# Optimization experiments

Hardware: AMD Instinct MI355X
Metric: run time of the kernel (lower is better)

## Reference

```python
import jax, jax.numpy as jnp
import numpy as np

B, L, H = 16, 2048, 768
V, D = 30000, 64


def setup_inputs() -> dict:
    key = jax.random.key(0)
    k1, k2, k3, k4 = jax.random.split(key, 4)
    bert_x = jax.random.normal(k1, (B, L, H), dtype=jnp.float32)
    x = jax.random.randint(k2, (B, L), 0, V, dtype=jnp.int64)
    ae = jax.random.normal(k3, (V, D), dtype=jnp.float32)
    w = jax.random.normal(k4, (D, D), dtype=jnp.float32)
    return {"bert_x": bert_x, "x": x, "ae": ae, "w": w}


def reference(bert_x, x, ae, w):
    # E[b,i] = ae[x[b,i]]  -> [B, L, D]
    E = ae[x]
    # fac[b,i,j] = E[b,i] @ w @ E[b,j]   (bilinear pairwise score)
    scores = jnp.einsum('bid,de,bje->bij', E, w, E)
    Lseq = bert_x.shape[1]
    i = jnp.arange(Lseq, dtype=bert_x.dtype)[:, None]
    j = jnp.arange(Lseq, dtype=bert_x.dtype)[None, :]
    # strictly-causal weight (i+1)/(j+1) for i < j, zero elsewhere
    coef = jnp.where(i < j, (i + 1.0) / (j + 1.0), 0.0).astype(bert_x.dtype)
    # res[:, j] = bert_x[:, j] + sum_{i<j} bert_x[:, i] * coef[i,j] * fac[b,i,j]
    res = bert_x + jnp.einsum('bij,bih->bjh', scores * coef, bert_x)
    return res
```

## Files before the change

kernel.cpp:

```cpp
#include <hip/hip_runtime.h>

#define Bb 16
#define Ll 2048
#define Hh 768
#define Dd 64
#define Cc 64
#define HC 64
#define NT (Hh / HC)
#define NCH (Ll / Cc)
#define NG 6

typedef __attribute__((ext_vector_type(8))) short bf16x8;
typedef __attribute__((ext_vector_type(4))) float f32x4;

__device__ __forceinline__ short f2bf(float f) {
  union { float f; unsigned u; } c;
  c.f = f;
  unsigned r = (c.u + 0x7FFFu + ((c.u >> 16) & 1u)) >> 16;
  return (short)r;
}
__device__ __forceinline__ unsigned pack2(float a, float b) {
  return (unsigned)(unsigned short)f2bf(a) | ((unsigned)(unsigned short)f2bf(b) << 16);
}
__device__ __forceinline__ float bf2f(unsigned short s) {
  union { unsigned u; float f; } c;
  c.u = ((unsigned)s) << 16;
  return c.f;
}

__device__ __forceinline__ void sync_lds() {
  asm volatile("s_waitcnt lgkmcnt(0)\n\ts_barrier" ::: "memory");
}

__global__ __launch_bounds__(512) void prep_kernel(const int* __restrict__ x,
                                                   const float* __restrict__ ae,
                                                   const float* __restrict__ w,
                                                   const float* __restrict__ bx,
                                                   short* __restrict__ Eg,
                                                   short* __restrict__ scTg,
                                                   short* __restrict__ Sch) {
  const int tid = threadIdx.x;
  const int wv = tid >> 6, lane = tid & 63, quad = lane >> 4, lq = lane & 15;
  const int mt = wv >> 1, np = wv & 1;
  const int b = blockIdx.x >> 5, ch = blockIdx.x & 31;
  const size_t gb = (size_t)blockIdx.x * 4096;
  __shared__ short pool[4 * 4096];
  short* sE  = pool;
  short* sWT = pool + 4096;
  short* sF  = pool + 8192;
  short* sFT = pool + 12288;

  {
    const int i = tid >> 3, seg = tid & 7;
    const int idx = x[b * Ll + ch * Cc + i];
    const float4* aer = (const float4*)(ae + (size_t)idx * Dd) + seg * 2;
    const float4 a0 = aer[0], a1 = aer[1];
    uint4 p;
    p.x = pack2(a0.x, a0.y); p.y = pack2(a0.z, a0.w);
    p.z = pack2(a1.x, a1.y); p.w = pack2(a1.z, a1.w);
    *(uint4*)&sE[i * 64 + ((seg ^ (i & 7)) << 3)] = p;
    *(uint4*)(Eg + gb + i * 64 + seg * 8) = p;
    const float4* wr = (const float4*)w;
#pragma unroll
    for (int q = 0; q < 2; ++q) {
      const int fl = q * 512 + tid;
      const int d = fl >> 4, es = (fl & 15) * 4;
      const float4 v = wr[fl];
      const float vv[4] = {v.x, v.y, v.z, v.w};
#pragma unroll
      for (int c = 0; c < 4; ++c) {
        const int e = es + c;
        sWT[e * 64 + (((d >> 3) ^ (e & 7)) << 3) + (d & 7)] = f2bf(vv[c]);
      }
    }
  }
  __syncthreads();

  const int rm = mt * 16 + lq;
  bf16x8 aE[2], aW[2];
#pragma unroll
  for (int ks = 0; ks < 2; ++ks) {
    const int blk = ((ks * 4 + quad) ^ (rm & 7)) << 3;
    aE[ks] = *(const bf16x8*)&sE[rm * 64 + blk];
    aW[ks] = *(const bf16x8*)&sWT[rm * 64 + blk];
  }

#pragma unroll
  for (int t = 0; t < 2; ++t) {
    const int nt = np * 2 + t;
    const int rn = nt * 16 + lq;
    f32x4 accF = {}, accT = {};
#pragma unroll
    for (int ks = 0; ks < 2; ++ks) {
      const int blk = ((ks * 4 + quad) ^ (rn & 7)) << 3;
      const bf16x8 bW = *(const bf16x8*)&sWT[rn * 64 + blk];
      const bf16x8 bE = *(const bf16x8*)&sE[rn * 64 + blk];
      accF = __builtin_amdgcn_mfma_f32_16x16x32_bf16(aE[ks], bW, accF, 0, 0, 0);
      accT = __builtin_amdgcn_mfma_f32_16x16x32_bf16(aW[ks], bE, accT, 0, 0, 0);
    }
#pragma unroll
    for (int r = 0; r < 4; ++r) {
      const int i = mt * 16 + quad * 4 + r;
      const int e = nt * 16 + lq;
      sF[i * 64 + (((e >> 3) ^ (i & 7)) << 3) + (e & 7)] = f2bf(accF[r]);
      const int d2 = mt * 16 + quad * 4 + r;
      const int i2 = nt * 16 + lq;
      sFT[d2 * 64 + (((i2 >> 3) ^ (d2 & 7)) << 3) + (i2 & 7)] = f2bf(accT[r]);
    }
  }
  __syncthreads();

  const int ip = tid & 31, hg = tid >> 5;
  float4 rGa[2], rGb[2];
  auto load_G = [&](int g) {
    const float* xr = bx + ((size_t)(b * Ll) + ch * Cc + 2 * ip) * Hh + g * 128 + hg * 8;
    rGa[0] = *(const float4*)(xr);
    rGa[1] = *(const float4*)(xr + 4);
    rGb[0] = *(const float4*)(xr + Hh);
    rGb[1] = *(const float4*)(xr + Hh + 4);
  };
  load_G(0);

#pragma unroll
  for (int t = 0; t < 2; ++t) {
    const int nt = np * 2 + t;
    const int rn = nt * 16 + lq;
    f32x4 acc = {};
#pragma unroll
    for (int ks = 0; ks < 2; ++ks) {
      const int blk = ((ks * 4 + quad) ^ (rn & 7)) << 3;
      const bf16x8 bF = *(const bf16x8*)&sF[rn * 64 + blk];
      acc = __builtin_amdgcn_mfma_f32_16x16x32_bf16(aE[ks], bF, acc, 0, 0, 0);
    }
#pragma unroll
    for (int r = 0; r < 4; ++r) {
      const int j = mt * 16 + quad * 4 + r;
      const int i = nt * 16 + lq;
      scTg[gb + j * 64 + i] = f2bf(i < j ? acc[r] : 0.f);
    }
  }

  bf16x8 bFT[4][2];
#pragma unroll
  for (int nt = 0; nt < 4; ++nt) {
    const int rn = nt * 16 + lq;
#pragma unroll
    for (int ks = 0; ks < 2; ++ks) {
      const int blk = ((ks * 4 + quad) ^ (rn & 7)) << 3;
      bFT[nt][ks] = *(const bf16x8*)&sFT[rn * 64 + blk];
    }
  }

  short* So = Sch + (size_t)blockIdx.x * (Hh * Dd);
#pragma unroll 2
  for (int g = 0; g < NG; ++g) {
    short* gbuf = pool + (g & 1) * 8192;
    {
      const float s0 = (float)(ch * Cc + 2 * ip + 1), s1 = (float)(ch * Cc + 2 * ip + 2);
      const float A[8] = {rGa[0].x, rGa[0].y, rGa[0].z, rGa[0].w,
                          rGa[1].x, rGa[1].y, rGa[1].z, rGa[1].w};
      const float Bv[8] = {rGb[0].x, rGb[0].y, rGb[0].z, rGb[0].w,
                           rGb[1].x, rGb[1].y, rGb[1].z, rGb[1].w};
#pragma unroll
      for (int e = 0; e < 8; ++e) {
        const int hl = hg * 8 + e;
        const int sa = hl * 64 + (((ip >> 2) ^ (hl & 7)) << 3) + 2 * (ip & 3);
        *(unsigned*)&gbuf[sa] = pack2(A[e] * s0, Bv[e] * s1);
      }
    }
    if (g + 1 < NG) load_G(g + 1);
    sync_lds();
    const int rh = wv * 16 + lq;
    bf16x8 aG[2];
#pragma unroll
    for (int ks = 0; ks < 2; ++ks) {
      const int blk = ((ks * 4 + quad) ^ (rh & 7)) << 3;
      aG[ks] = *(const bf16x8*)&gbuf[rh * 64 + blk];
    }
#pragma unroll
    for (int nt = 0; nt < 4; ++nt) {
      f32x4 acc = {};
#pragma unroll
      for (int ks = 0; ks < 2; ++ks)
        acc = __builtin_amdgcn_mfma_f32_16x16x32_bf16(aG[ks], bFT[nt][ks], acc, 0, 0, 0);
#pragma unroll
      for (int r = 0; r < 4; ++r) {
        const int h = g * 128 + wv * 16 + quad * 4 + r;
        So[h * 64 + nt * 16 + lq] = f2bf(acc[r]);
      }
    }
  }
}

__global__ __launch_bounds__(256) void prefix_kernel(short* __restrict__ Sch) {
  const int b = blockIdx.x / 48;
  const int v = (blockIdx.x % 48) * 256 + threadIdx.x;
  uint2* base = (uint2*)(Sch + (size_t)b * NCH * (Hh * Dd)) + v;
  const int stride = Hh * Dd / 4;
  uint2 va[NCH];
#pragma unroll
  for (int s = 0; s < NCH; ++s) va[s] = base[s * stride];
  float4 acc = {0.f, 0.f, 0.f, 0.f};
#pragma unroll
  for (int s = 0; s < NCH; ++s) {
    uint2 o;
    o.x = pack2(acc.x, acc.y);
    o.y = pack2(acc.z, acc.w);
    base[s * stride] = o;
    acc.x += bf2f((unsigned short)(va[s].x & 0xffffu));
    acc.y += bf2f((unsigned short)(va[s].x >> 16));
    acc.z += bf2f((unsigned short)(va[s].y & 0xffffu));
    acc.w += bf2f((unsigned short)(va[s].y >> 16));
  }
}

__global__ __launch_bounds__(256) void scan_kernel(const float* __restrict__ bx,
                                                   const short* __restrict__ Eg,
                                                   const short* __restrict__ scTg,
                                                   const short* __restrict__ STg,
                                                   float* __restrict__ out) {
  const int s = blockIdx.x;
  const int tile = s >> 9;
  const int bc = s & 511;
  const int b = bc >> 5, ch = bc & 31;
  const int tid = threadIdx.x;
  const int w = tid >> 6, lane = tid & 63, quad = lane >> 4, lq = lane & 15;
  const int ip = tid & 31, hg = tid >> 5;
  const int rj = w * 16 + lq;

  __shared__ short sGT[64 * 64];

  float4 rGa[2], rGb[2];
  {
    const float* xr = bx + ((size_t)(b * Ll) + ch * Cc + 2 * ip) * Hh + tile * HC + hg * 8;
    rGa[0] = *(const float4*)(xr);
    rGa[1] = *(const float4*)(xr + 4);
    rGb[0] = *(const float4*)(xr + Hh);
    rGb[1] = *(const float4*)(xr + Hh + 4);
  }
  bf16x8 aC1[2], aC2[2];
  {
    const size_t tb = (size_t)bc * 4096;
#pragma unroll
    for (int ks = 0; ks < 2; ++ks) {
      const int o = rj * 64 + (ks * 4 + quad) * 8;
      aC1[ks] = *(const bf16x8*)(scTg + tb + o);
      aC2[ks] = *(const bf16x8*)(Eg + tb + o);
    }
  }
  bf16x8 stF[4][2];
  {
    const short* Sp = STg + (size_t)bc * (Hh * Dd);
#pragma unroll
    for (int ht = 0; ht < 4; ++ht) {
      const int h = tile * HC + ht * 16 + lq;
#pragma unroll
      for (int ks = 0; ks < 2; ++ks)
        stF[ht][ks] = *(const bf16x8*)(Sp + h * 64 + (ks * 4 + quad) * 8);
    }
  }

  {
    const float s0 = (float)(ch * Cc + 2 * ip + 1), s1 = (float)(ch * Cc + 2 * ip + 2);
    const float A[8] = {rGa[0].x, rGa[0].y, rGa[0].z, rGa[0].w,
                        rGa[1].x, rGa[1].y, rGa[1].z, rGa[1].w};
    const float Bv[8] = {rGb[0].x, rGb[0].y, rGb[0].z, rGb[0].w,
                         rGb[1].x, rGb[1].y, rGb[1].z, rGb[1].w};
#pragma unroll
    for (int e = 0; e < 8; ++e) {
      const int hl = hg * 8 + e;
      const int sa = hl * 64 + (((ip >> 2) ^ (hl & 7)) << 3) + 2 * (ip & 3);
      *(unsigned*)&sGT[sa] = pack2(A[e] * s0, Bv[e] * s1);
    }
  }
  sync_lds();

#pragma unroll
  for (int ht = 0; ht < 4; ++ht) {
    const int rh = ht * 16 + lq;
    f32x4 accO = {};
#pragma unroll
    for (int ks = 0; ks < 2; ++ks) {
      const int blk = ((ks * 4 + quad) ^ (rh & 7)) << 3;
      const bf16x8 gv = *(const bf16x8*)&sGT[rh * 64 + blk];
      accO = __builtin_amdgcn_mfma_f32_16x16x32_bf16(aC1[ks], gv, accO, 0, 0, 0);
      accO = __builtin_amdgcn_mfma_f32_16x16x32_bf16(aC2[ks], stF[ht][ks], accO, 0, 0, 0);
    }
#pragma unroll
    for (int r = 0; r < 4; ++r) {
      const int gj = ch * Cc + w * 16 + quad * 4 + r;
      const size_t off = ((size_t)(b * Ll) + gj) * Hh + tile * HC + ht * 16 + lq;
      out[off] = bx[off] + accO[r] * (1.0f / (float)(gj + 1));
    }
  }
}

extern "C" void kernel_launch(void* const* d_in, const int* in_sizes, int n_in,
                              void* d_out, int out_size, void* d_ws, size_t ws_size,
                              hipStream_t stream) {
  (void)in_sizes; (void)n_in; (void)out_size; (void)ws_size;
  const float* bx = (const float*)d_in[0];
  const int* x = (const int*)d_in[1];
  const float* ae = (const float*)d_in[2];
  const float* w = (const float*)d_in[3];
  float* out = (float*)d_out;
  short* Eg = (short*)d_ws;
  short* scTg = Eg + (size_t)512 * 4096;
  short* Sch = scTg + (size_t)512 * 4096;

  prep_kernel<<<Bb * NCH, 512, 0, stream>>>(x, ae, w, bx, Eg, scTg, Sch);
  prefix_kernel<<<Bb * 48, 256, 0, stream>>>(Sch);
  scan_kernel<<<NT * Bb * NCH, 256, 0, stream>>>(bx, Eg, scTg, Sch, out);
}
```

Measured before the change: 263.9 us.

## Process four H-tiles per scan block with double-buffered LDS and prefetch

Each scan_kernel block now loops over four consecutive 64-wide H tiles instead of one. The per-chunk A-operand fragments (scTg, Eg) are loaded once and reused across the tiles. The next tile's bert_x and prefix-state loads are issued while the current tile computes, with the LDS staging buffer alternating between two copies. This cuts the grid by four and removes redundant operand loads, but it lowers block-level parallelism and raises register and LDS use per block.

```diff
diff --git a/kernel.cpp b/kernel.cpp
--- a/kernel.cpp
+++ b/kernel.cpp
@@ -9,6 +9,8 @@
 #define NT (Hh / HC)
 #define NCH (Ll / Cc)
 #define NG 6
+#define TG 4
+#define NTG (NT / TG)
 
 typedef __attribute__((ext_vector_type(8))) short bf16x8;
 typedef __attribute__((ext_vector_type(4))) float f32x4;
@@ -220,7 +222,7 @@
                                                    const short* __restrict__ STg,
                                                    float* __restrict__ out) {
   const int s = blockIdx.x;
-  const int tile = s >> 9;
+  const int tg = s >> 9;
   const int bc = s & 511;
   const int b = bc >> 5, ch = bc & 31;
   const int tid = threadIdx.x;
@@ -228,70 +230,82 @@
   const int ip = tid & 31, hg = tid >> 5;
   const int rj = w * 16 + lq;
 
-  __shared__ short sGT[64 * 64];
+  __shared__ short sGT[2][64 * 64];
+
+  bf16x8 aC1[2], aC2[2];
+  {
+    const size_t tb = (size_t)bc * 4096;
+#pragma unroll
+    for (int ks = 0; ks < 2; ++ks) {
+      const int o = rj * 64 + (ks * 4 + quad) * 8;
+      aC1[ks] = *(const bf16x8*)(scTg + tb + o);
+      aC2[ks] = *(const bf16x8*)(Eg + tb + o);
+    }
+  }
+  const short* Sp = STg + (size_t)bc * (Hh * Dd);
 
   float4 rGa[2], rGb[2];
-  {
-    const float* xr = bx + ((size_t)(b * Ll) + ch * Cc + 2 * ip) * Hh + tile * HC + hg * 8;
+  bf16x8 stF[4][2];
+  auto load_G = [&](int tl) {
+    const float* xr = bx + ((size_t)(b * Ll) + ch * Cc + 2 * ip) * Hh + tl * HC + hg * 8;
     rGa[0] = *(const float4*)(xr);
     rGa[1] = *(const float4*)(xr + 4);
     rGb[0] = *(const float4*)(xr + Hh);
     rGb[1] = *(const float4*)(xr + Hh + 4);
-  }
-  bf16x8 aC1[2], aC2[2];
-  {
-    const size_t tb = (size_t)bc * 4096;
-#pragma unroll
-    for (int ks = 0; ks < 2; ++ks) {
-      const int o = rj * 64 + (ks * 4 + quad) * 8;
-      aC1[ks] = *(const bf16x8*)(scTg + tb + o);
-      aC2[ks] = *(const bf16x8*)(Eg + tb + o);
-    }
-  }
-  bf16x8 stF[4][2];
-  {
-    const short* Sp = STg + (size_t)bc * (Hh * Dd);
+  };
+  auto load_S = [&](int tl) {
 #pragma unroll
     for (int ht = 0; ht < 4; ++ht) {
-      const int h = tile * HC + ht * 16 + lq;
+      const int h = tl * HC + ht * 16 + lq;
 #pragma unroll
       for (int ks = 0; ks < 2; ++ks)
         stF[ht][ks] = *(const bf16x8*)(Sp + h * 64 + (ks * 4 + quad) * 8);
     }
-  }
-
-  {
-    const float s0 = (float)(ch * Cc + 2 * ip + 1), s1 = (float)(ch * Cc + 2 * ip + 2);
-    const float A[8] = {rGa[0].x, rGa[0].y, rGa[0].z, rGa[0].w,
-                        rGa[1].x, rGa[1].y, rGa[1].z, rGa[1].w};
-    const float Bv[8] = {rGb[0].x, rGb[0].y, rGb[0].z, rGb[0].w,
-                         rGb[1].x, rGb[1].y, rGb[1].z, rGb[1].w};
-#pragma unroll
-    for (int e = 0; e < 8; ++e) {
-      const int hl = hg * 8 + e;
-      const int sa = hl * 64 + (((ip >> 2) ^ (hl & 7)) << 3) + 2 * (ip & 3);
-      *(unsigned*)&sGT[sa] = pack2(A[e] * s0, Bv[e] * s1);
-    }
-  }
-  sync_lds();
-
-#pragma unroll
-  for (int ht = 0; ht < 4; ++ht) {
-    const int rh = ht * 16 + lq;
-    f32x4 accO = {};
-#pragma unroll
-    for (int ks = 0; ks < 2; ++ks) {
-      const int blk = ((ks * 4 + quad) ^ (rh & 7)) << 3;
-      const bf16x8 gv = *(const bf16x8*)&sGT[rh * 64 + blk];
-      accO = __builtin_amdgcn_mfma_f32_16x16x32_bf16(aC1[ks], gv, accO, 0, 0, 0);
-      accO = __builtin_amdgcn_mfma_f32_16x16x32_bf16(aC2[ks], stF[ht][ks], accO, 0, 0, 0);
-    }
-#pragma unroll
-    for (int r = 0; r < 4; ++r) {
-      const int gj = ch * Cc + w * 16 + quad * 4 + r;
-      const size_t off = ((size_t)(b * Ll) + gj) * Hh + tile * HC + ht * 16 + lq;
-      out[off] = bx[off] + accO[r] * (1.0f / (float)(gj + 1));
-    }
+  };
+
+  load_G(tg * TG);
+  load_S(tg * TG);
+
+  const float s0 = (float)(ch * Cc + 2 * ip + 1), s1 = (float)(ch * Cc + 2 * ip + 2);
+
+#pragma unroll
+  for (int t = 0; t < TG; ++t) {
+    const int tl = tg * TG + t;
+    short* gbuf = sGT[t & 1];
+    {
+      const float A[8] = {rGa[0].x, rGa[0].y, rGa[0].z, rGa[0].w,
+                          rGa[1].x, rGa[1].y, rGa[1].z, rGa[1].w};
+      const float Bv[8] = {rGb[0].x, rGb[0].y, rGb[0].z, rGb[0].w,
+                           rGb[1].x, rGb[1].y, rGb[1].z, rGb[1].w};
+#pragma unroll
+      for (int e = 0; e < 8; ++e) {
+        const int hl = hg * 8 + e;
+        const int sa = hl * 64 + (((ip >> 2) ^ (hl & 7)) << 3) + 2 * (ip & 3);
+        *(unsigned*)&gbuf[sa] = pack2(A[e] * s0, Bv[e] * s1);
+      }
+    }
+    if (t + 1 < TG) load_G(tl + 1);
+    sync_lds();
+
+#pragma unroll
+    for (int ht = 0; ht < 4; ++ht) {
+      const int rh = ht * 16 + lq;
+      f32x4 accO = {};
+#pragma unroll
+      for (int ks = 0; ks < 2; ++ks) {
+        const int blk = ((ks * 4 + quad) ^ (rh & 7)) << 3;
+        const bf16x8 gv = *(const bf16x8*)&gbuf[rh * 64 + blk];
+        accO = __builtin_amdgcn_mfma_f32_16x16x32_bf16(aC1[ks], gv, accO, 0, 0, 0);
+        accO = __builtin_amdgcn_mfma_f32_16x16x32_bf16(aC2[ks], stF[ht][ks], accO, 0, 0, 0);
+      }
+#pragma unroll
+      for (int r = 0; r < 4; ++r) {
+        const int gj = ch * Cc + w * 16 + quad * 4 + r;
+        const size_t off = ((size_t)(b * Ll) + gj) * Hh + tl * HC + ht * 16 + lq;
+        out[off] = bx[off] + accO[r] * (1.0f / (float)(gj + 1));
+      }
+    }
+    if (t + 1 < TG) load_S(tl + 1);
   }
 }
 
@@ -310,5 +324,5 @@
 
   prep_kernel<<<Bb * NCH, 512, 0, stream>>>(x, ae, w, bx, Eg, scTg, Sch);
   prefix_kernel<<<Bb * 48, 256, 0, stream>>>(Sch);
-  scan_kernel<<<NT * Bb * NCH, 256, 0, stream>>>(bx, Eg, scTg, Sch, out);
-}
+  scan_kernel<<<NTG * Bb * NCH, 256, 0, stream>>>(bx, Eg, scTg, Sch, out);
+}
```

After: 259.9 us. No clear change (-1.5%).

## Fuse prep, prefix and scan kernels into one kernel with per-batch grid barriers

Applied to the files above, without the earlier changes.

Merges the three launches into a single persistent-style kernel of 512 blocks. Per-batch atomic counter barriers separate the chunk-state computation, the cross-chunk prefix sum and the output pass. E and the masked score tile stay in LDS instead of round-tripping through global memory, and the output pass loops over H tiles with prefetch of the next state fragments. The barrier assumes all 32 blocks of a batch are co-resident; the spin has a timeout but could deadlock or silently break correctness. It also adds a memset launch and lowers parallelism in the output phase.

```diff
diff --git a/kernel.cpp b/kernel.cpp
--- a/kernel.cpp
+++ b/kernel.cpp
@@ -5,10 +5,8 @@
 #define Hh 768
 #define Dd 64
 #define Cc 64
-#define HC 64
-#define NT (Hh / HC)
-#define NCH (Ll / Cc)
-#define NG 6
+#define NCH 32
+#define NTL 12
 
 typedef __attribute__((ext_vector_type(8))) short bf16x8;
 typedef __attribute__((ext_vector_type(4))) float f32x4;
@@ -32,23 +30,41 @@
   asm volatile("s_waitcnt lgkmcnt(0)\n\ts_barrier" ::: "memory");
 }
 
-__global__ __launch_bounds__(512) void prep_kernel(const int* __restrict__ x,
-                                                   const float* __restrict__ ae,
-                                                   const float* __restrict__ w,
-                                                   const float* __restrict__ bx,
-                                                   short* __restrict__ Eg,
-                                                   short* __restrict__ scTg,
-                                                   short* __restrict__ Sch) {
+__device__ __forceinline__ void batch_barrier(unsigned* c) {
+  __syncthreads();
+  if (threadIdx.x == 0) {
+    __threadfence();
+    atomicAdd(c, 1u);
+    unsigned it = 0;
+    while (atomicAdd(c, 0u) < 32u) {
+      __builtin_amdgcn_s_sleep(8);
+      if (++it > (1u << 21)) break;
+    }
+  }
+  __syncthreads();
+  __threadfence();
+}
+
+__global__ __launch_bounds__(512, 4) void fused_kernel(const int* __restrict__ x,
+                                                       const float* __restrict__ ae,
+                                                       const float* __restrict__ w,
+                                                       const float* __restrict__ bx,
+                                                       short* __restrict__ Sch,
+                                                       unsigned* __restrict__ cnt,
+                                                       float* __restrict__ out) {
   const int tid = threadIdx.x;
   const int wv = tid >> 6, lane = tid & 63, quad = lane >> 4, lq = lane & 15;
   const int mt = wv >> 1, np = wv & 1;
-  const int b = blockIdx.x >> 5, ch = blockIdx.x & 31;
-  const size_t gb = (size_t)blockIdx.x * 4096;
-  __shared__ short pool[4 * 4096];
-  short* sE  = pool;
-  short* sWT = pool + 4096;
-  short* sF  = pool + 8192;
-  short* sFT = pool + 12288;
+  const int bc = blockIdx.x;
+  const int b = bc >> 5, ch = bc & 31;
+  const int ip = tid & 31, hg = tid >> 5;
+
+  __shared__ short lds[20480];
+  short* sE   = lds;
+  short* sWT  = lds + 4096;
+  short* sF   = lds + 8192;
+  short* sFT  = lds + 12288;
+  short* sScT = lds + 16384;
 
   {
     const int i = tid >> 3, seg = tid & 7;
@@ -59,7 +75,6 @@
     p.x = pack2(a0.x, a0.y); p.y = pack2(a0.z, a0.w);
     p.z = pack2(a1.x, a1.y); p.w = pack2(a1.z, a1.w);
     *(uint4*)&sE[i * 64 + ((seg ^ (i & 7)) << 3)] = p;
-    *(uint4*)(Eg + gb + i * 64 + seg * 8) = p;
     const float4* wr = (const float4*)w;
 #pragma unroll
     for (int q = 0; q < 2; ++q) {
@@ -110,16 +125,24 @@
   }
   __syncthreads();
 
-  const int ip = tid & 31, hg = tid >> 5;
-  float4 rGa[2], rGb[2];
+  float4 rGa, rGb;
   auto load_G = [&](int g) {
-    const float* xr = bx + ((size_t)(b * Ll) + ch * Cc + 2 * ip) * Hh + g * 128 + hg * 8;
-    rGa[0] = *(const float4*)(xr);
-    rGa[1] = *(const float4*)(xr + 4);
-    rGb[0] = *(const float4*)(xr + Hh);
-    rGb[1] = *(const float4*)(xr + Hh + 4);
+    const float* xr = bx + ((size_t)(b * Ll) + ch * Cc + 2 * ip) * Hh + g * 64 + hg * 4;
+    rGa = *(const float4*)xr;
+    rGb = *(const float4*)(xr + Hh);
   };
   load_G(0);
+  const float s0 = (float)(ch * Cc + 2 * ip + 1), s1 = s0 + 1.0f;
+  auto stage_G = [&](short* gbuf) {
+    const float A[4] = {rGa.x, rGa.y, rGa.z, rGa.w};
+    const float Bv[4] = {rGb.x, rGb.y, rGb.z, rGb.w};
+#pragma unroll
+    for (int e = 0; e < 4; ++e) {
+      const int hl = hg * 4 + e;
+      const int sa = hl * 64 + (((ip >> 2) ^ (hl & 7)) << 3) + 2 * (ip & 3);
+      *(unsigned*)&gbuf[sa] = pack2(A[e] * s0, Bv[e] * s1);
+    }
+  };
 
 #pragma unroll
   for (int t = 0; t < 2; ++t) {
@@ -136,161 +159,136 @@
     for (int r = 0; r < 4; ++r) {
       const int j = mt * 16 + quad * 4 + r;
       const int i = nt * 16 + lq;
-      scTg[gb + j * 64 + i] = f2bf(i < j ? acc[r] : 0.f);
-    }
-  }
-
-  bf16x8 bFT[4][2];
-#pragma unroll
-  for (int nt = 0; nt < 4; ++nt) {
-    const int rn = nt * 16 + lq;
+      sScT[j * 64 + i] = f2bf(i < j ? acc[r] : 0.f);
+    }
+  }
+
+  bf16x8 bFT[2][2];
+#pragma unroll
+  for (int tl = 0; tl < 2; ++tl) {
+    const int rn = ((wv >> 2) * 2 + tl) * 16 + lq;
 #pragma unroll
     for (int ks = 0; ks < 2; ++ks) {
       const int blk = ((ks * 4 + quad) ^ (rn & 7)) << 3;
-      bFT[nt][ks] = *(const bf16x8*)&sFT[rn * 64 + blk];
-    }
-  }
-
-  short* So = Sch + (size_t)blockIdx.x * (Hh * Dd);
+      bFT[tl][ks] = *(const bf16x8*)&sFT[rn * 64 + blk];
+    }
+  }
+
+  short* So = Sch + (size_t)bc * (Hh * Dd);
 #pragma unroll 2
-  for (int g = 0; g < NG; ++g) {
-    short* gbuf = pool + (g & 1) * 8192;
-    {
-      const float s0 = (float)(ch * Cc + 2 * ip + 1), s1 = (float)(ch * Cc + 2 * ip + 2);
-      const float A[8] = {rGa[0].x, rGa[0].y, rGa[0].z, rGa[0].w,
-                          rGa[1].x, rGa[1].y, rGa[1].z, rGa[1].w};
-      const float Bv[8] = {rGb[0].x, rGb[0].y, rGb[0].z, rGb[0].w,
-                           rGb[1].x, rGb[1].y, rGb[1].z, rGb[1].w};
-#pragma unroll
-      for (int e = 0; e < 8; ++e) {
-        const int hl = hg * 8 + e;
-        const int sa = hl * 64 + (((ip >> 2) ^ (hl & 7)) << 3) + 2 * (ip & 3);
-        *(unsigned*)&gbuf[sa] = pack2(A[e] * s0, Bv[e] * s1);
-      }
-    }
-    if (g + 1 < NG) load_G(g + 1);
+  for (int g = 0; g < NTL; ++g) {
+    short* gbuf = lds + 4096 + (g & 1) * 4096;
+    stage_G(gbuf);
+    if (g + 1 < NTL) load_G(g + 1);
     sync_lds();
-    const int rh = wv * 16 + lq;
+    const int rh = (wv & 3) * 16 + lq;
     bf16x8 aG[2];
 #pragma unroll
-    for (int ks = 0; ks < 2; ++ks) {
-      const int blk = ((ks * 4 + quad) ^ (rh & 7)) << 3;
-      aG[ks] = *(const bf16x8*)&gbuf[rh * 64 + blk];
-    }
-#pragma unroll
-    for (int nt = 0; nt < 4; ++nt) {
+    for (int ks = 0; ks < 2; ++ks)
+      aG[ks] = *(const bf16x8*)&gbuf[rh * 64 + (((ks * 4 + quad) ^ (rh & 7)) << 3)];
+#pragma unroll
+    for (int tl = 0; tl < 2; ++tl) {
       f32x4 acc = {};
 #pragma unroll
       for (int ks = 0; ks < 2; ++ks)
-        acc = __builtin_amdgcn_mfma_f32_16x16x32_bf16(aG[ks], bFT[nt][ks], acc, 0, 0, 0);
+        acc = __builtin_amdgcn_mfma_f32_16x16x32_bf16(aG[ks], bFT[tl][ks], acc, 0, 0, 0);
+      const int nt = (wv >> 2) * 2 + tl;
 #pragma unroll
       for (int r = 0; r < 4; ++r) {
-        const int h = g * 128 + wv * 16 + quad * 4 + r;
+        const int h = g * 64 + (wv & 3) * 16 + quad * 4 + r;
         So[h * 64 + nt * 16 + lq] = f2bf(acc[r]);
       }
     }
   }
-}
-
-__global__ __launch_bounds__(256) void prefix_kernel(short* __restrict__ Sch) {
-  const int b = blockIdx.x / 48;
-  const int v = (blockIdx.x % 48) * 256 + threadIdx.x;
-  uint2* base = (uint2*)(Sch + (size_t)b * NCH * (Hh * Dd)) + v;
-  const int stride = Hh * Dd / 4;
-  uint2 va[NCH];
-#pragma unroll
-  for (int s = 0; s < NCH; ++s) va[s] = base[s * stride];
-  float4 acc = {0.f, 0.f, 0.f, 0.f};
-#pragma unroll
-  for (int s = 0; s < NCH; ++s) {
-    uint2 o;
-    o.x = pack2(acc.x, acc.y);
-    o.y = pack2(acc.z, acc.w);
-    base[s * stride] = o;
-    acc.x += bf2f((unsigned short)(va[s].x & 0xffffu));
-    acc.y += bf2f((unsigned short)(va[s].x >> 16));
-    acc.z += bf2f((unsigned short)(va[s].y & 0xffffu));
-    acc.w += bf2f((unsigned short)(va[s].y >> 16));
-  }
-}
-
-__global__ __launch_bounds__(256) void scan_kernel(const float* __restrict__ bx,
-                                                   const short* __restrict__ Eg,
-                                                   const short* __restrict__ scTg,
-                                                   const short* __restrict__ STg,
-                                                   float* __restrict__ out) {
-  const int s = blockIdx.x;
-  const int tile = s >> 9;
-  const int bc = s & 511;
-  const int b = bc >> 5, ch = bc & 31;
-  const int tid = threadIdx.x;
-  const int w = tid >> 6, lane = tid & 63, quad = lane >> 4, lq = lane & 15;
-  const int ip = tid & 31, hg = tid >> 5;
-  const int rj = w * 16 + lq;
-
-  __shared__ short sGT[64 * 64];
-
-  float4 rGa[2], rGb[2];
+
+  batch_barrier(&cnt[b]);
+
   {
-    const float* xr = bx + ((size_t)(b * Ll) + ch * Cc + 2 * ip) * Hh + tile * HC + hg * 8;
-    rGa[0] = *(const float4*)(xr);
-    rGa[1] = *(const float4*)(xr + 4);
-    rGb[0] = *(const float4*)(xr + Hh);
-    rGb[1] = *(const float4*)(xr + Hh + 4);
-  }
+    const int col = ch * 512 + tid;
+    if (col < (Hh * Dd / 4)) {
+      uint2* base = (uint2*)Sch + (size_t)b * NCH * (Hh * Dd / 4) + col;
+      const int stride = Hh * Dd / 4;
+      float4 acc = {0.f, 0.f, 0.f, 0.f};
+#pragma unroll
+      for (int hf = 0; hf < 2; ++hf) {
+        uint2 va[16];
+#pragma unroll
+        for (int s = 0; s < 16; ++s) va[s] = base[(hf * 16 + s) * stride];
+#pragma unroll
+        for (int s = 0; s < 16; ++s) {
+          uint2 o;
+          o.x = pack2(acc.x, acc.y);
+          o.y = pack2(acc.z, acc.w);
+          base[(hf * 16 + s) * stride] = o;
+          acc.x += bf2f((unsigned short)(va[s].x & 0xffffu));
+          acc.y += bf2f((unsigned short)(va[s].x >> 16));
+          acc.z += bf2f((unsigned short)(va[s].y & 0xffffu));
+          acc.w += bf2f((unsigned short)(va[s].y >> 16));
+        }
+      }
+    }
+  }
+
+  batch_barrier(&cnt[16 + b]);
+
+  const int jt = wv & 3, hth = wv >> 2;
+  const int rj = jt * 16 + lq;
   bf16x8 aC1[2], aC2[2];
-  {
-    const size_t tb = (size_t)bc * 4096;
-#pragma unroll
-    for (int ks = 0; ks < 2; ++ks) {
-      const int o = rj * 64 + (ks * 4 + quad) * 8;
-      aC1[ks] = *(const bf16x8*)(scTg + tb + o);
-      aC2[ks] = *(const bf16x8*)(Eg + tb + o);
-    }
-  }
-  bf16x8 stF[4][2];
-  {
-    const short* Sp = STg + (size_t)bc * (Hh * Dd);
-#pragma unroll
-    for (int ht = 0; ht < 4; ++ht) {
-      const int h = tile * HC + ht * 16 + lq;
+#pragma unroll
+  for (int ks = 0; ks < 2; ++ks) {
+    aC1[ks] = *(const bf16x8*)&sScT[rj * 64 + (ks * 4 + quad) * 8];
+    aC2[ks] = *(const bf16x8*)&sE[rj * 64 + (((ks * 4 + quad) ^ (rj & 7)) << 3)];
+  }
+  const short* Sp = Sch + (size_t)bc * (Hh * Dd);
+  float inv[4];
+  size_t rowb[4];
+#pragma unroll
+  for (int r = 0; r < 4; ++r) {
+    const int gj = ch * Cc + jt * 16 + quad * 4 + r;
+    inv[r] = 1.0f / (float)(gj + 1);
+    rowb[r] = ((size_t)(b * Ll) + gj) * Hh;
+  }
+  bf16x8 stC[2][2], stN[2][2];
+  auto load_S = [&](int t, bf16x8 st[2][2]) {
+#pragma unroll
+    for (int k = 0; k < 2; ++k) {
+      const int h = t * 64 + (hth * 2 + k) * 16 + lq;
 #pragma unroll
       for (int ks = 0; ks < 2; ++ks)
-        stF[ht][ks] = *(const bf16x8*)(Sp + h * 64 + (ks * 4 + quad) * 8);
-    }
-  }
-
-  {
-    const float s0 = (float)(ch * Cc + 2 * ip + 1), s1 = (float)(ch * Cc + 2 * ip + 2);
-    const float A[8] = {rGa[0].x, rGa[0].y, rGa[0].z, rGa[0].w,
-                        rGa[1].x, rGa[1].y, rGa[1].z, rGa[1].w};
-    const float Bv[8] = {rGb[0].x, rGb[0].y, rGb[0].z, rGb[0].w,
-                         rGb[1].x, rGb[1].y, rGb[1].z, rGb[1].w};
-#pragma unroll
-    for (int e = 0; e < 8; ++e) {
-      const int hl = hg * 8 + e;
-      const int sa = hl * 64 + (((ip >> 2) ^ (hl & 7)) << 3) + 2 * (ip & 3);
-      *(unsigned*)&sGT[sa] = pack2(A[e] * s0, Bv[e] * s1);
-    }
-  }
-  sync_lds();
-
-#pragma unroll
-  for (int ht = 0; ht < 4; ++ht) {
-    const int rh = ht * 16 + lq;
-    f32x4 accO = {};
-#pragma unroll
-    for (int ks = 0; ks < 2; ++ks) {
-      const int blk = ((ks * 4 + quad) ^ (rh & 7)) << 3;
-      const bf16x8 gv = *(const bf16x8*)&sGT[rh * 64 + blk];
-      accO = __builtin_amdgcn_mfma_f32_16x16x32_bf16(aC1[ks], gv, accO, 0, 0, 0);
-      accO = __builtin_amdgcn_mfma_f32_16x16x32_bf16(aC2[ks], stF[ht][ks], accO, 0, 0, 0);
-    }
-#pragma unroll
-    for (int r = 0; r < 4; ++r) {
-      const int gj = ch * Cc + w * 16 + quad * 4 + r;
-      const size_t off = ((size_t)(b * Ll) + gj) * Hh + tile * HC + ht * 16 + lq;
-      out[off] = bx[off] + accO[r] * (1.0f / (float)(gj + 1));
+        st[k][ks] = *(const bf16x8*)(Sp + h * 64 + (ks * 4 + quad) * 8);
+    }
+  };
+  load_G(0);
+  load_S(0, stC);
+#pragma unroll
+  for (int t = 0; t < NTL; ++t) {
+    short* gbuf = lds + 4096 + (t & 1) * 4096;
+    stage_G(gbuf);
+    if (t + 1 < NTL) load_G(t + 1);
+    sync_lds();
+#pragma unroll
+    for (int k = 0; k < 2; ++k) {
+      const int rh = (hth * 2 + k) * 16 + lq;
+      f32x4 accO = {};
+#pragma unroll
+      for (int ks = 0; ks < 2; ++ks) {
+        const bf16x8 gv = *(const bf16x8*)&gbuf[rh * 64 + (((ks * 4 + quad) ^ (rh & 7)) << 3)];
+        accO = __builtin_amdgcn_mfma_f32_16x16x32_bf16(aC1[ks], gv, accO, 0, 0, 0);
+        accO = __builtin_amdgcn_mfma_f32_16x16x32_bf16(aC2[ks], stC[k][ks], accO, 0, 0, 0);
+      }
+      const int hcol = t * 64 + (hth * 2 + k) * 16 + lq;
+#pragma unroll
+      for (int r = 0; r < 4; ++r) {
+        const size_t off = rowb[r] + hcol;
+        out[off] = bx[off] + accO[r] * inv[r];
+      }
+    }
+    if (t + 1 < NTL) {
+      load_S(t + 1, stN);
+#pragma unroll
+      for (int k = 0; k < 2; ++k)
+#pragma unroll
+        for (int ks = 0; ks < 2; ++ks) stC[k][ks] = stN[k][ks];
     }
   }
 }
@@ -304,11 +302,9 @@
   const float* ae = (const float*)d_in[2];
   const float* w = (const float*)d_in[3];
   float* out = (float*)d_out;
-  short* Eg = (short*)d_ws;
-  short* scTg = Eg + (size_t)512 * 4096;
-  short* Sch = scTg + (size_t)512 * 4096;
-
-  prep_kernel<<<Bb * NCH, 512, 0, stream>>>(x, ae, w, bx, Eg, scTg, Sch);
-  prefix_kernel<<<Bb * 48, 256, 0, stream>>>(Sch);
-  scan_kernel<<<NT * Bb * NCH, 256, 0, stream>>>(bx, Eg, scTg, Sch, out);
-}
+  short* Sch = (short*)d_ws;
+  unsigned* cnt = (unsigned*)(Sch + (size_t)512 * Hh * Dd);
+
+  hipMemsetAsync(cnt, 0, 128, stream);
+  fused_kernel<<<Bb * NCH, 512, 0, stream>>>(x, ae, w, bx, Sch, cnt, out);
+}
```

Result: slower. 583.0 us (+120.9%).
